# Performance work log

Hardware: AMD Instinct MI355X
Metric: run time of the kernel (lower is better)

## Reference

```python
import math
import jax, jax.numpy as jnp
import numpy as np

B, T, C, NH = 2, 2048, 2048, 16
HD = C // NH  # 128


def _quantize_int6(key, out_f, in_f):
    """Replicates Int6LinearDynamic.reset_parameters/_quantize_update."""
    w = jax.random.normal(key, (out_f, in_f), jnp.float32) * (1.0 / math.sqrt(in_f))
    max_val = jnp.clip(jnp.max(jnp.abs(w), axis=1, keepdims=True), 1e-5)
    scale = max_val / 31.0
    w_int = jnp.clip(jnp.round(w / scale), -32, 31).astype(jnp.int8)
    return w_int, scale.squeeze(1)  # [out,in] int8, [out] f32


def setup_inputs() -> dict:
    key = jax.random.key(0)
    k_x, k_a, k_p = jax.random.split(key, 3)
    attn_w, attn_scales = _quantize_int6(k_a, 3 * C, C)
    proj_w, proj_scales = _quantize_int6(k_p, C, C)
    return {
        "x": jax.random.normal(k_x, (B, T, C), jnp.float32),
        "attn_w": attn_w,
        "attn_scales": attn_scales,
        "proj_w": proj_w,
        "proj_scales": proj_scales,
        "qk_gain": jnp.float32(1.0),
    }


def _l2norm(t):
    # F.normalize(p=2, dim=-1, eps=1e-12)
    n = jnp.sqrt(jnp.sum(t * t, axis=-1, keepdims=True))
    return t / jnp.maximum(n, 1e-12)


def reference(x, attn_w, attn_scales, proj_w, proj_scales, qk_gain):
    # dequantized int6 GEMM: w = int8 * per-row scale
    wa = attn_w.astype(jnp.float32) * attn_scales[:, None]  # [3C, C]
    qkv = jnp.einsum("btc,oc->bto", x, wa)                   # [B,T,3C]
    q, k, v = jnp.split(qkv, 3, axis=2)

    def heads(t):  # [B,T,C] -> [B,NH,T,HD]
        return t.reshape(B, T, NH, HD).transpose(0, 2, 1, 3)

    q, k, v = heads(q), heads(k), heads(v)
    q = _l2norm(q) * qk_gain
    k = _l2norm(k) * qk_gain

    # causal SDPA, default scale 1/sqrt(head_dim)
    scores = jnp.einsum("bhqd,bhkd->bhqk", q, k) / math.sqrt(HD)
    causal = jnp.tril(jnp.ones((T, T), dtype=bool))
    scores = jnp.where(causal, scores, -jnp.inf)
    attn = jax.nn.softmax(scores, axis=-1)
    y = jnp.einsum("bhqk,bhkd->bhqd", attn, v)               # [B,NH,T,HD]
    y = y.transpose(0, 2, 1, 3).reshape(B, T, C)

    wp = proj_w.astype(jnp.float32) * proj_scales[:, None]   # [C, C]
    return jnp.einsum("btc,oc->bto", y, wp)
```

## Files before the change

kernel.cpp:

```cpp
#include <hip/hip_runtime.h>


#define DEVINL __device__ __forceinline__

typedef unsigned short u16;
typedef __bf16 bf16x8 __attribute__((ext_vector_type(8)));
typedef float  f32x4  __attribute__((ext_vector_type(4)));
typedef float  f32x16 __attribute__((ext_vector_type(16)));
typedef short  short8 __attribute__((ext_vector_type(8)));
typedef u16    u16x4  __attribute__((ext_vector_type(4)));
typedef unsigned uint4x __attribute__((ext_vector_type(4)));

static constexpr int T_  = 2048;
static constexpr int C_  = 2048;
static constexpr int TC3 = 6144;

DEVINL u16 f2bf(float f) {
  union { float f; unsigned u; } v; v.f = f;
  unsigned r = v.u + 0x7FFFu + ((v.u >> 16) & 1u);
  return (u16)(r >> 16);
}
DEVINL float bf2f(u16 s) {
  union { unsigned u; float f; } v; v.u = ((unsigned)s) << 16;
  return v.f;
}
DEVINL bf16x8 ld8(const u16* p) {
  return __builtin_bit_cast(bf16x8, *(const short8*)p);
}
DEVINL f32x4 mfma16(bf16x8 a, bf16x8 b, f32x4 c) {
  return __builtin_amdgcn_mfma_f32_16x16x32_bf16(a, b, c, 0, 0, 0);
}
DEVINL f32x16 mfma32(bf16x8 a, bf16x8 b, f32x16 c) {
  return __builtin_amdgcn_mfma_f32_32x32x16_bf16(a, b, c, 0, 0, 0);
}
DEVINL void async_cp16(const u16* gp, u16* lp) {
  __builtin_amdgcn_global_load_lds(
      (const __attribute__((address_space(1))) void*)gp,
      (__attribute__((address_space(3))) void*)lp, 16, 0, 0);
}
DEVINL unsigned cvtpk(float lo, float hi) {
  unsigned r;
  asm("v_cvt_pk_bf16_f32 %0, %1, %2" : "=v"(r) : "v"(lo), "v"(hi));
  return r;
}
DEVINL void plswap(unsigned& a, unsigned& b) {
  asm("v_permlane32_swap_b32 %0, %1" : "+v"(a), "+v"(b));
}
template<int N> DEVINL void vmwait() {
  if constexpr (N == 0)      asm volatile("s_waitcnt vmcnt(0)" ::: "memory");
  else if constexpr (N == 5) asm volatile("s_waitcnt vmcnt(5)" ::: "memory");
  else if constexpr (N == 7) asm volatile("s_waitcnt vmcnt(7)" ::: "memory");
  else if constexpr (N == 9) asm volatile("s_waitcnt vmcnt(9)" ::: "memory");
}

__global__ __launch_bounds__(256) void k_cast_x(const float* __restrict__ in,
                                                u16* __restrict__ out) {
  long i = (long)(blockIdx.x * 256 + threadIdx.x) * 4;
  float4 v = *(const float4*)(in + i);
  u16x4 o; o.x = f2bf(v.x); o.y = f2bf(v.y); o.z = f2bf(v.z); o.w = f2bf(v.w);
  *(u16x4*)(out + i) = o;
}
__global__ __launch_bounds__(256) void k_cast_w(const int* __restrict__ in,
                                                u16* __restrict__ out) {
  long i = (long)(blockIdx.x * 256 + threadIdx.x) * 4;
  int4 v = *(const int4*)(in + i);
  u16x4 o; o.x = f2bf((float)v.x); o.y = f2bf((float)v.y);
  o.z = f2bf((float)v.z); o.w = f2bf((float)v.w);
  *(u16x4*)(out + i) = o;
}

template<bool OUT_BF16>
__global__ __launch_bounds__(256) void k_gemm_bt(
    const u16* __restrict__ A, const u16* __restrict__ Bt,
    const float* __restrict__ scale, void* __restrict__ Cv,
    int N, long K) {
  __shared__ u16 As[128 * 32];
  __shared__ u16 Bs[128 * 32];
  const int tid  = threadIdx.x;
  const int wave = tid >> 6;
  const int lane = tid & 63;
  const int l15  = lane & 15;
  const int quad = lane >> 4;
  const int wm = (wave & 1) * 64;
  const int wn = (wave >> 1) * 64;
  const long bm = (long)blockIdx.y * 128;
  const long bn = (long)blockIdx.x * 128;

  f32x4 acc[4][4] = {};

  const int srow = lane >> 2;
  const int scol = (lane & 3) * 8;

  for (long k0 = 0; k0 < K; k0 += 32) {
#pragma unroll
    for (int i = 0; i < 2; ++i) {
      const int j = wave * 2 + i;
      const int row = j * 16 + srow;
      async_cp16(A  + (bm + row) * K + k0 + scol, &As[j * 512]);
      async_cp16(Bt + (bn + row) * K + k0 + scol, &Bs[j * 512]);
    }
    __syncthreads();
    bf16x8 af[4], bfr[4];
#pragma unroll
    for (int mi = 0; mi < 4; ++mi)
      af[mi] = ld8(&As[(wm + mi * 16 + l15) * 32 + quad * 8]);
#pragma unroll
    for (int ni = 0; ni < 4; ++ni)
      bfr[ni] = ld8(&Bs[(wn + ni * 16 + l15) * 32 + quad * 8]);
#pragma unroll
    for (int mi = 0; mi < 4; ++mi)
#pragma unroll
      for (int ni = 0; ni < 4; ++ni)
        acc[mi][ni] = mfma16(af[mi], bfr[ni], acc[mi][ni]);
    __syncthreads();
  }
#pragma unroll
  for (int ni = 0; ni < 4; ++ni) {
    const long col = bn + wn + ni * 16 + l15;
    const float sc = scale[col];
#pragma unroll
    for (int mi = 0; mi < 4; ++mi) {
      const long row0 = bm + wm + mi * 16 + quad * 4;
#pragma unroll
      for (int r = 0; r < 4; ++r) {
        float v = acc[mi][ni][r] * sc;
        if constexpr (OUT_BF16) ((u16*)Cv)[(row0 + r) * (long)N + col] = f2bf(v);
        else                    ((float*)Cv)[(row0 + r) * (long)N + col] = v;
      }
    }
  }
}

template<int SZ>
DEVINL void stage_q(const u16* __restrict__ G, long brow, long K, int tt, int qi,
                    u16 (&L)[2][SZ], int w, int lane) {
  const int sr = w * 8 + (lane >> 3);
  const int sc = lane & 7;
  const long grow = brow + qi * 64 + sr;
  async_cp16(G + grow * K + (long)(tt << 6) + ((sc ^ (sr & 7)) << 3),
             &L[tt & 1][(qi * 64 + w * 8) * 64]);
}

template<int WP1, int WP3, bool ISS0, bool ISS123, bool LAST>
DEVINL void kstep256(int t, const u16* __restrict__ A, const u16* __restrict__ Bt,
                     long K, long bm, long bn,
                     u16 (&As)[2][256 * 64], u16 (&Bs)[2][192 * 64],
                     f32x4 (&acc)[8][3], int w, int lane) {
  const int l15 = lane & 15, quad = lane >> 4;
  const int wm = (w & 1) * 128;
  const int wn = (w >> 1) * 48;
  const int buf = t & 1;

  auto rdA = [&](int mi, int kc) -> bf16x8 {
    const int row = wm + mi * 16 + l15;
    const int k0 = kc * 32 + quad * 8;
    return ld8(&As[buf][row * 64 + (k0 ^ ((row & 7) * 8))]);
  };
  auto rdB = [&](int ni, int kc) -> bf16x8 {
    const int row = wn + ni * 16 + l15;
    const int k0 = kc * 32 + quad * 8;
    return ld8(&Bs[buf][row * 64 + (k0 ^ ((row & 7) * 8))]);
  };

  bf16x8 af[4][2], bfl[2][2];
#pragma unroll
  for (int mi = 0; mi < 4; ++mi) { af[mi][0] = rdA(mi, 0); af[mi][1] = rdA(mi, 1); }
#pragma unroll
  for (int ni = 0; ni < 2; ++ni) { bfl[ni][0] = rdB(ni, 0); bfl[ni][1] = rdB(ni, 1); }
  if constexpr (ISS0) {
    stage_q(A, bm, K, t + 1, 1, As, w, lane);
    stage_q(A, bm, K, t + 1, 3, As, w, lane);
  }
  __builtin_amdgcn_s_barrier();
  __builtin_amdgcn_s_setprio(1);
#pragma unroll
  for (int mi = 0; mi < 4; ++mi)
#pragma unroll
    for (int ni = 0; ni < 2; ++ni) {
      acc[mi][ni] = mfma16(af[mi][0], bfl[ni][0], acc[mi][ni]);
      acc[mi][ni] = mfma16(af[mi][1], bfl[ni][1], acc[mi][ni]);
    }
  __builtin_amdgcn_s_setprio(0);
  __builtin_amdgcn_s_barrier();

  bf16x8 bfh[2];
  bfh[0] = rdB(2, 0); bfh[1] = rdB(2, 1);
  if constexpr (ISS123) {
    stage_q(A, bm, K, t + 2, 0, As, w, lane);
    stage_q(A, bm, K, t + 2, 2, As, w, lane);
  }
  __builtin_amdgcn_s_barrier();
  __builtin_amdgcn_s_setprio(1);
#pragma unroll
  for (int mi = 0; mi < 4; ++mi) {
    acc[mi][2] = mfma16(af[mi][0], bfh[0], acc[mi][2]);
    acc[mi][2] = mfma16(af[mi][1], bfh[1], acc[mi][2]);
  }
  __builtin_amdgcn_s_setprio(0);
  vmwait<WP1>();
  __builtin_amdgcn_s_barrier();

  bf16x8 af2[4][2];
#pragma unroll
  for (int mi = 0; mi < 4; ++mi) { af2[mi][0] = rdA(4 + mi, 0); af2[mi][1] = rdA(4 + mi, 1); }
  if constexpr (ISS123) {
    stage_q(Bt, bn, K, t + 2, 0, Bs, w, lane);
    stage_q(Bt, bn, K, t + 2, 1, Bs, w, lane);
  }
  __builtin_amdgcn_s_barrier();
  __builtin_amdgcn_s_setprio(1);
#pragma unroll
  for (int mi = 0; mi < 4; ++mi) {
    acc[4 + mi][2] = mfma16(af2[mi][0], bfh[0], acc[4 + mi][2]);
    acc[4 + mi][2] = mfma16(af2[mi][1], bfh[1], acc[4 + mi][2]);
  }
  __builtin_amdgcn_s_setprio(0);
  __builtin_amdgcn_s_barrier();

  if constexpr (ISS123) {
    stage_q(Bt, bn, K, t + 2, 2, Bs, w, lane);
  }
  __builtin_amdgcn_s_setprio(1);
#pragma unroll
  for (int mi = 0; mi < 4; ++mi)
#pragma unroll
    for (int ni = 0; ni < 2; ++ni) {
      acc[4 + mi][ni] = mfma16(af2[mi][0], bfl[ni][0], acc[4 + mi][ni]);
      acc[4 + mi][ni] = mfma16(af2[mi][1], bfl[ni][1], acc[4 + mi][ni]);
    }
  __builtin_amdgcn_s_setprio(0);
  if constexpr (!LAST) {
    vmwait<WP3>();
    __builtin_amdgcn_s_barrier();
  }
}

__global__ __launch_bounds__(512, 2) void k_gemm256(
    const u16* __restrict__ A, const u16* __restrict__ Bt,
    const float* __restrict__ scale, u16* __restrict__ C,
    int N, long K) {
  __shared__ u16 As[2][256 * 64];
  __shared__ u16 Bs[2][192 * 64];
  const int tid = threadIdx.x, w = tid >> 6, lane = tid & 63;
  const long bm = (long)blockIdx.y * 256;
  const long bn = (long)blockIdx.x * 192;
  const int nt = (int)(K >> 6);

  stage_q(A, bm, K, 0, 0, As, w, lane); stage_q(A, bm, K, 0, 2, As, w, lane);
  stage_q(Bt, bn, K, 0, 0, Bs, w, lane); stage_q(Bt, bn, K, 0, 1, Bs, w, lane);
  stage_q(Bt, bn, K, 0, 2, Bs, w, lane);
  stage_q(A, bm, K, 0, 1, As, w, lane); stage_q(A, bm, K, 0, 3, As, w, lane);
  stage_q(A, bm, K, 1, 0, As, w, lane); stage_q(A, bm, K, 1, 2, As, w, lane);
  stage_q(Bt, bn, K, 1, 0, Bs, w, lane); stage_q(Bt, bn, K, 1, 1, Bs, w, lane);
  stage_q(Bt, bn, K, 1, 2, Bs, w, lane);
  vmwait<5>();
  __builtin_amdgcn_s_barrier();

  f32x4 acc[8][3] = {};
  int t = 0;
  for (; t < nt - 2; ++t)
    kstep256<9, 5, true, true, false>(t, A, Bt, K, bm, bn, As, Bs, acc, w, lane);
  kstep256<7, 0, true, false, false>(nt - 2, A, Bt, K, bm, bn, As, Bs, acc, w, lane);
  kstep256<0, 0, false, false, true>(nt - 1, A, Bt, K, bm, bn, As, Bs, acc, w, lane);

  const int l15 = lane & 15, quad = lane >> 4;
  const int wm = (w & 1) * 128, wn = (w >> 1) * 48;
#pragma unroll
  for (int ni = 0; ni < 3; ++ni) {
    const long col = bn + wn + ni * 16 + l15;
    const float sc = scale[col];
#pragma unroll
    for (int mi = 0; mi < 8; ++mi) {
      const long row0 = bm + wm + mi * 16 + quad * 4;
#pragma unroll
      for (int r = 0; r < 4; ++r)
        C[(row0 + r) * (long)N + col] = f2bf(acc[mi][ni][r] * sc);
    }
  }
}

__global__ __launch_bounds__(256) void k_norm_qk(u16* __restrict__ qkv,
                                                 const float* __restrict__ qk_gain) {
  const int token = blockIdx.x;
  const int wave = threadIdx.x >> 6, lane = threadIdx.x & 63;
  const float g = qk_gain[0];
  const float qmul = g * g * 1.44269504f * 0.08838834764f;
  u16* rowp = qkv + (long)token * TC3;
#pragma unroll
  for (int s = 0; s < 8; ++s) {
    const int seg = wave * 8 + s;
    const int isK = seg >> 4;
    const int h = seg & 15;
    u16* ptr = rowp + isK * C_ + h * 128 + lane * 2;
    unsigned pv = *(const unsigned*)ptr;
    float a = bf2f((u16)(pv & 0xffffu));
    float bb = bf2f((u16)(pv >> 16));
    float ss = a * a + bb * bb;
#pragma unroll
    for (int m = 1; m <= 32; m <<= 1) ss += __shfl_xor(ss, m);
    float denom = fmaxf(sqrtf(ss), 1e-12f);
    float f = (isK ? 1.0f : qmul) / denom;
    u16 o0 = f2bf(a * f), o1 = f2bf(bb * f);
    *(unsigned*)ptr = (unsigned)o0 | ((unsigned)o1 << 16);
  }
}

__global__ __launch_bounds__(256) void k_vt(const u16* __restrict__ qkv,
                                            u16* __restrict__ vt) {
  const int t0 = blockIdx.x * 64;
  const int h = blockIdx.y, bz = blockIdx.z;
  const int t = threadIdx.x & 63;
  const int d0 = threadIdx.x >> 6;
  const long tokbase = (long)bz * T_;
  const u16* src = qkv + (tokbase + t0 + t) * (long)TC3 + 2 * C_ + h * 128;
  u16* dst = vt + ((long)(bz * 16 + h) * 128) * (long)T_ + t0 + t;
#pragma unroll
  for (int dd = 0; dd < 32; ++dd) {
    const int d = dd * 4 + d0;
    dst[(long)d * T_] = src[d];
  }
}

__global__ __launch_bounds__(256, 2) void k_attn(const u16* __restrict__ qkv,
                                                 const u16* __restrict__ vtg,
                                                 u16* __restrict__ y) {
  const int qt = blockIdx.z ? (15 - blockIdx.x) : blockIdx.x;
  const int h  = blockIdx.y;
  const int bz = blockIdx.z;
  const int tid = threadIdx.x, w = tid >> 6, lane = tid & 63;
  const int m31 = lane & 31, hi = lane >> 5;

  __shared__ u16 Ks[2][64 * 128];
  __shared__ u16 Vt[2][128 * 64];

  const long tokbase = (long)bz * T_;
  const int qbase = qt * 128 + w * 32;
  const u16* vbase = vtg + ((long)(bz * 16 + h) * 128) * (long)T_;
  const u16* kbase = qkv + tokbase * TC3 + C_ + h * 128;

  bf16x8 qf[8];
  {
    const u16* qp = qkv + (tokbase + qbase + m31) * (long)TC3 + h * 128 + hi * 8;
#pragma unroll
    for (int kc = 0; kc < 8; ++kc)
      qf[kc] = ld8(qp + kc * 16);
  }

  f32x16 o[4];
#pragma unroll
  for (int i = 0; i < 4; ++i)
#pragma unroll
    for (int r = 0; r < 16; ++r) o[i][r] = 0.f;
  f32x4 lacc = {0.f, 0.f, 0.f, 0.f};

  auto stage = [&](int ktb, int b) {
#pragma unroll
    for (int j = 0; j < 4; ++j) {
      const int t = w * 4 + j;
      const int p = t * 64 + lane;
      const int r  = p >> 4, ck = p & 15;
      async_cp16(kbase + (long)(ktb + r) * TC3 + ((ck ^ (r & 15)) * 8),
                 &Ks[b][t * 512]);
      const int d  = p >> 3, cv = p & 7;
      async_cp16(vbase + (long)d * T_ + ktb + ((cv ^ (d & 7)) * 8),
                 &Vt[b][t * 512]);
    }
  };

  stage(0, 0);
  __syncthreads();
  int b = 0;
  const int ktmax = 2 * qt + 1;

  for (int kt = 0; kt <= ktmax; ++kt) {
    const int ktb = kt * 64;
    if (kt < ktmax) stage(ktb + 64, b ^ 1);

    if (ktb <= qbase + 31) {
      f32x16 sA[2];
      __builtin_amdgcn_s_setprio(1);
#pragma unroll
      for (int kb = 0; kb < 2; ++kb) {
        f32x16 acc;
#pragma unroll
        for (int r = 0; r < 16; ++r) acc[r] = 0.f;
#pragma unroll
        for (int kc = 0; kc < 8; ++kc) {
          bf16x8 kf = ld8(&Ks[b][(kb * 32 + m31) * 128 +
                                 (((2 * kc + hi) ^ (lane & 15)) * 8)]);
          acc = mfma32(kf, qf[kc], acc);
        }
        sA[kb] = acc;
      }
      __builtin_amdgcn_s_setprio(0);

      if (ktb + 63 > qbase) {
        const int qq = qbase + m31;
#pragma unroll
        for (int kb = 0; kb < 2; ++kb)
#pragma unroll
          for (int r = 0; r < 16; ++r) {
            const int key = ktb + kb * 32 + (r & 3) + 8 * (r >> 2) + 4 * hi;
            if (key > qq) sA[kb][r] = -1e30f;
          }
      }
#pragma unroll
      for (int kb = 0; kb < 2; ++kb)
#pragma unroll
        for (int r = 0; r < 16; ++r) {
          float p = __builtin_amdgcn_exp2f(sA[kb][r]);
          sA[kb][r] = p;
          lacc[r & 3] += p;
        }

      bf16x8 pb[4];
#pragma unroll
      for (int ks = 0; ks < 4; ++ks) {
        const int kb = ks >> 1, j = ks & 1;
        unsigned w0a = cvtpk(sA[kb][8 * j + 0], sA[kb][8 * j + 1]);
        unsigned w1a = cvtpk(sA[kb][8 * j + 2], sA[kb][8 * j + 3]);
        unsigned w0b = cvtpk(sA[kb][8 * j + 4], sA[kb][8 * j + 5]);
        unsigned w1b = cvtpk(sA[kb][8 * j + 6], sA[kb][8 * j + 7]);
        plswap(w0a, w0b);
        plswap(w1a, w1b);
        uint4x t; t.x = w0a; t.y = w1a; t.z = w0b; t.w = w1b;
        pb[ks] = __builtin_bit_cast(bf16x8, t);
      }

      __builtin_amdgcn_s_setprio(1);
#pragma unroll
      for (int db = 0; db < 4; ++db)
#pragma unroll
        for (int ks = 0; ks < 4; ++ks) {
          bf16x8 vf = ld8(&Vt[b][(db * 32 + m31) * 64 +
                                 (((2 * ks + hi) ^ (m31 & 7)) * 8)]);
          o[db] = mfma32(vf, pb[ks], o[db]);
        }
      __builtin_amdgcn_s_setprio(0);
    }

    if (kt < ktmax) __syncthreads();
    b ^= 1;
  }

  float lrow = lacc[0] + lacc[1] + lacc[2] + lacc[3];
  lrow += __shfl_xor(lrow, 32);
  const float inv_l = 1.0f / lrow;
  u16* yp = y + (tokbase + qbase + m31) * (long)C_ + h * 128 + 4 * hi;
#pragma unroll
  for (int db = 0; db < 4; ++db)
#pragma unroll
    for (int g = 0; g < 4; ++g) {
      u16x4 pk;
#pragma unroll
      for (int r = 0; r < 4; ++r) pk[r] = f2bf(o[db][g * 4 + r] * inv_l);
      *(u16x4*)(yp + db * 32 + g * 8) = pk;
    }
}

extern "C" void kernel_launch(void* const* d_in, const int* in_sizes, int n_in,
                              void* d_out, int out_size, void* d_ws, size_t ws_size,
                              hipStream_t stream) {
  const float* x    = (const float*)d_in[0];
  const int*   aw   = (const int*)d_in[1];
  const float* asc  = (const float*)d_in[2];
  const int*   pw   = (const int*)d_in[3];
  const float* psc  = (const float*)d_in[4];
  const float* gain = (const float*)d_in[5];

  char* ws = (char*)d_ws;
  u16* xb  = (u16*)(ws);
  u16* wab = (u16*)(ws + 16777216UL);
  u16* wpb = (u16*)(ws + 41943040UL);
  u16* qkv = (u16*)(ws + 50331648UL);
  u16* yb  = (u16*)(ws + 100663296UL);
  u16* vtg = xb;

  k_cast_x<<<8192, 256, 0, stream>>>(x, xb);
  k_cast_w<<<12288, 256, 0, stream>>>(aw, wab);
  k_cast_w<<<4096, 256, 0, stream>>>(pw, wpb);
  k_gemm256<<<dim3(32, 16), 512, 0, stream>>>(xb, wab, asc, qkv, TC3, (long)C_);
  k_norm_qk<<<4096, 256, 0, stream>>>(qkv, gain);
  k_vt<<<dim3(32, 16, 2), 256, 0, stream>>>(qkv, vtg);
  k_attn<<<dim3(16, 16, 2), 256, 0, stream>>>(qkv, vtg, yb);
  k_gemm_bt<false><<<dim3(16, 32), 256, 0, stream>>>(yb, wpb, psc, (float*)d_out, C_, (long)C_);
}
```

Baseline: 419.4 us.

## Merge cast and norm/transpose launches; add pipelined 128x256 projection GEMM

Folds the three cast kernels into one launch and the q/k normalisation and V transpose into another, cutting launch count. It also replaces the simple 128x128, K=32 projection GEMM with a 512-thread, 128x256-tile kernel. The new kernel double-buffers 64-wide K slices in swizzled LDS via async copies and interleaves MFMA sub-blocks with barriers and setprio. The costs are more LDS per block (96 KB, double-buffered) and a more complex barrier schedule.

New measurement: 416.3 us. Within noise of the previous version (-0.7%).

```diff
diff --git a/kernel.cpp b/kernel.cpp
--- a/kernel.cpp
+++ b/kernel.cpp
@@ -53,81 +53,25 @@
   else if constexpr (N == 9) asm volatile("s_waitcnt vmcnt(9)" ::: "memory");
 }
 
-__global__ __launch_bounds__(256) void k_cast_x(const float* __restrict__ in,
-                                                u16* __restrict__ out) {
-  long i = (long)(blockIdx.x * 256 + threadIdx.x) * 4;
-  float4 v = *(const float4*)(in + i);
-  u16x4 o; o.x = f2bf(v.x); o.y = f2bf(v.y); o.z = f2bf(v.z); o.w = f2bf(v.w);
-  *(u16x4*)(out + i) = o;
-}
-__global__ __launch_bounds__(256) void k_cast_w(const int* __restrict__ in,
-                                                u16* __restrict__ out) {
-  long i = (long)(blockIdx.x * 256 + threadIdx.x) * 4;
-  int4 v = *(const int4*)(in + i);
-  u16x4 o; o.x = f2bf((float)v.x); o.y = f2bf((float)v.y);
-  o.z = f2bf((float)v.z); o.w = f2bf((float)v.w);
-  *(u16x4*)(out + i) = o;
-}
-
-template<bool OUT_BF16>
-__global__ __launch_bounds__(256) void k_gemm_bt(
-    const u16* __restrict__ A, const u16* __restrict__ Bt,
-    const float* __restrict__ scale, void* __restrict__ Cv,
-    int N, long K) {
-  __shared__ u16 As[128 * 32];
-  __shared__ u16 Bs[128 * 32];
-  const int tid  = threadIdx.x;
-  const int wave = tid >> 6;
-  const int lane = tid & 63;
-  const int l15  = lane & 15;
-  const int quad = lane >> 4;
-  const int wm = (wave & 1) * 64;
-  const int wn = (wave >> 1) * 64;
-  const long bm = (long)blockIdx.y * 128;
-  const long bn = (long)blockIdx.x * 128;
-
-  f32x4 acc[4][4] = {};
-
-  const int srow = lane >> 2;
-  const int scol = (lane & 3) * 8;
-
-  for (long k0 = 0; k0 < K; k0 += 32) {
-#pragma unroll
-    for (int i = 0; i < 2; ++i) {
-      const int j = wave * 2 + i;
-      const int row = j * 16 + srow;
-      async_cp16(A  + (bm + row) * K + k0 + scol, &As[j * 512]);
-      async_cp16(Bt + (bn + row) * K + k0 + scol, &Bs[j * 512]);
-    }
-    __syncthreads();
-    bf16x8 af[4], bfr[4];
-#pragma unroll
-    for (int mi = 0; mi < 4; ++mi)
-      af[mi] = ld8(&As[(wm + mi * 16 + l15) * 32 + quad * 8]);
-#pragma unroll
-    for (int ni = 0; ni < 4; ++ni)
-      bfr[ni] = ld8(&Bs[(wn + ni * 16 + l15) * 32 + quad * 8]);
-#pragma unroll
-    for (int mi = 0; mi < 4; ++mi)
-#pragma unroll
-      for (int ni = 0; ni < 4; ++ni)
-        acc[mi][ni] = mfma16(af[mi], bfr[ni], acc[mi][ni]);
-    __syncthreads();
-  }
-#pragma unroll
-  for (int ni = 0; ni < 4; ++ni) {
-    const long col = bn + wn + ni * 16 + l15;
-    const float sc = scale[col];
-#pragma unroll
-    for (int mi = 0; mi < 4; ++mi) {
-      const long row0 = bm + wm + mi * 16 + quad * 4;
-#pragma unroll
-      for (int r = 0; r < 4; ++r) {
-        float v = acc[mi][ni][r] * sc;
-        if constexpr (OUT_BF16) ((u16*)Cv)[(row0 + r) * (long)N + col] = f2bf(v);
-        else                    ((float*)Cv)[(row0 + r) * (long)N + col] = v;
-      }
-    }
+__global__ __launch_bounds__(256) void k_cast_all(
+    const float* __restrict__ x, const int* __restrict__ aw,
+    const int* __restrict__ pw, u16* __restrict__ xb,
+    u16* __restrict__ wab, u16* __restrict__ wpb) {
+  const int b = blockIdx.x;
+  if (b < 8192) {
+    long i = (long)(b * 256 + threadIdx.x) * 4;
+    float4 v = *(const float4*)(x + i);
+    u16x4 o; o.x = f2bf(v.x); o.y = f2bf(v.y); o.z = f2bf(v.z); o.w = f2bf(v.w);
+    *(u16x4*)(xb + i) = o;
+  } else {
+    const int* in; u16* out; int lb;
+    if (b < 20480) { in = aw; out = wab; lb = b - 8192; }
+    else           { in = pw; out = wpb; lb = b - 20480; }
+    long i = (long)(lb * 256 + threadIdx.x) * 4;
+    int4 v = *(const int4*)(in + i);
+    u16x4 o; o.x = f2bf((float)v.x); o.y = f2bf((float)v.y);
+    o.z = f2bf((float)v.z); o.w = f2bf((float)v.w);
+    *(u16x4*)(out + i) = o;
   }
 }
 
@@ -279,45 +223,167 @@
   }
 }
 
-__global__ __launch_bounds__(256) void k_norm_qk(u16* __restrict__ qkv,
-                                                 const float* __restrict__ qk_gain) {
-  const int token = blockIdx.x;
-  const int wave = threadIdx.x >> 6, lane = threadIdx.x & 63;
-  const float g = qk_gain[0];
-  const float qmul = g * g * 1.44269504f * 0.08838834764f;
-  u16* rowp = qkv + (long)token * TC3;
-#pragma unroll
-  for (int s = 0; s < 8; ++s) {
-    const int seg = wave * 8 + s;
-    const int isK = seg >> 4;
-    const int h = seg & 15;
-    u16* ptr = rowp + isK * C_ + h * 128 + lane * 2;
-    unsigned pv = *(const unsigned*)ptr;
-    float a = bf2f((u16)(pv & 0xffffu));
-    float bb = bf2f((u16)(pv >> 16));
-    float ss = a * a + bb * bb;
-#pragma unroll
-    for (int m = 1; m <= 32; m <<= 1) ss += __shfl_xor(ss, m);
-    float denom = fmaxf(sqrtf(ss), 1e-12f);
-    float f = (isK ? 1.0f : qmul) / denom;
-    u16 o0 = f2bf(a * f), o1 = f2bf(bb * f);
-    *(unsigned*)ptr = (unsigned)o0 | ((unsigned)o1 << 16);
-  }
-}
-
-__global__ __launch_bounds__(256) void k_vt(const u16* __restrict__ qkv,
-                                            u16* __restrict__ vt) {
-  const int t0 = blockIdx.x * 64;
-  const int h = blockIdx.y, bz = blockIdx.z;
-  const int t = threadIdx.x & 63;
-  const int d0 = threadIdx.x >> 6;
-  const long tokbase = (long)bz * T_;
-  const u16* src = qkv + (tokbase + t0 + t) * (long)TC3 + 2 * C_ + h * 128;
-  u16* dst = vt + ((long)(bz * 16 + h) * 128) * (long)T_ + t0 + t;
-#pragma unroll
-  for (int dd = 0; dd < 32; ++dd) {
-    const int d = dd * 4 + d0;
-    dst[(long)d * T_] = src[d];
+__global__ __launch_bounds__(512, 2) void k_gemm_proj(
+    const u16* __restrict__ A, const u16* __restrict__ Bt,
+    const float* __restrict__ scale, float* __restrict__ C,
+    int N, long K) {
+  __shared__ u16 As[2][128 * 64];
+  __shared__ u16 Bs[2][256 * 64];
+  const int tid = threadIdx.x, w = tid >> 6, lane = tid & 63;
+  const int l15 = lane & 15, quad = lane >> 4;
+  const int wm = (w & 1) * 64, wn = (w >> 1) * 64;
+  const long bm = (long)blockIdx.y * 128;
+  const long bn = (long)blockIdx.x * 256;
+  const int nt = (int)(K >> 6);
+
+  auto rdA = [&](int mi, int kc, int buf) -> bf16x8 {
+    const int row = wm + mi * 16 + l15;
+    const int k0 = kc * 32 + quad * 8;
+    return ld8(&As[buf][row * 64 + (k0 ^ ((row & 7) * 8))]);
+  };
+  auto rdB = [&](int ni, int kc, int buf) -> bf16x8 {
+    const int row = wn + ni * 16 + l15;
+    const int k0 = kc * 32 + quad * 8;
+    return ld8(&Bs[buf][row * 64 + (k0 ^ ((row & 7) * 8))]);
+  };
+
+  stage_q(A, bm, K, 0, 0, As, w, lane); stage_q(A, bm, K, 0, 1, As, w, lane);
+  stage_q(Bt, bn, K, 0, 0, Bs, w, lane); stage_q(Bt, bn, K, 0, 1, Bs, w, lane);
+  stage_q(Bt, bn, K, 0, 2, Bs, w, lane); stage_q(Bt, bn, K, 0, 3, Bs, w, lane);
+  vmwait<0>();
+  __builtin_amdgcn_s_barrier();
+
+  f32x4 acc[4][4] = {};
+  for (int t = 0; t < nt; ++t) {
+    const int buf = t & 1;
+    const bool iss = (t < nt - 1);
+    bf16x8 a01[2][2], a23[2][2], b01[2][2], b23[2][2];
+
+    if (iss) {
+      stage_q(Bt, bn, K, t + 1, 0, Bs, w, lane);
+      stage_q(Bt, bn, K, t + 1, 1, Bs, w, lane);
+      stage_q(A,  bm, K, t + 1, 0, As, w, lane);
+    }
+#pragma unroll
+    for (int mi = 0; mi < 2; ++mi) { a01[mi][0] = rdA(mi, 0, buf); a01[mi][1] = rdA(mi, 1, buf); }
+#pragma unroll
+    for (int ni = 0; ni < 2; ++ni) { b01[ni][0] = rdB(ni, 0, buf); b01[ni][1] = rdB(ni, 1, buf); }
+    __builtin_amdgcn_s_barrier();
+    __builtin_amdgcn_s_setprio(1);
+#pragma unroll
+    for (int mi = 0; mi < 2; ++mi)
+#pragma unroll
+      for (int ni = 0; ni < 2; ++ni) {
+        acc[mi][ni] = mfma16(a01[mi][0], b01[ni][0], acc[mi][ni]);
+        acc[mi][ni] = mfma16(a01[mi][1], b01[ni][1], acc[mi][ni]);
+      }
+    __builtin_amdgcn_s_setprio(0);
+    __builtin_amdgcn_s_barrier();
+
+    if (iss) {
+      stage_q(Bt, bn, K, t + 1, 2, Bs, w, lane);
+      stage_q(Bt, bn, K, t + 1, 3, Bs, w, lane);
+      stage_q(A,  bm, K, t + 1, 1, As, w, lane);
+    }
+#pragma unroll
+    for (int ni = 0; ni < 2; ++ni) { b23[ni][0] = rdB(2 + ni, 0, buf); b23[ni][1] = rdB(2 + ni, 1, buf); }
+    __builtin_amdgcn_s_barrier();
+    __builtin_amdgcn_s_setprio(1);
+#pragma unroll
+    for (int mi = 0; mi < 2; ++mi)
+#pragma unroll
+      for (int ni = 0; ni < 2; ++ni) {
+        acc[mi][2 + ni] = mfma16(a01[mi][0], b23[ni][0], acc[mi][2 + ni]);
+        acc[mi][2 + ni] = mfma16(a01[mi][1], b23[ni][1], acc[mi][2 + ni]);
+      }
+    __builtin_amdgcn_s_setprio(0);
+    __builtin_amdgcn_s_barrier();
+
+#pragma unroll
+    for (int mi = 0; mi < 2; ++mi) { a23[mi][0] = rdA(2 + mi, 0, buf); a23[mi][1] = rdA(2 + mi, 1, buf); }
+    __builtin_amdgcn_s_barrier();
+    __builtin_amdgcn_s_setprio(1);
+#pragma unroll
+    for (int mi = 0; mi < 2; ++mi)
+#pragma unroll
+      for (int ni = 0; ni < 2; ++ni) {
+        acc[2 + mi][2 + ni] = mfma16(a23[mi][0], b23[ni][0], acc[2 + mi][2 + ni]);
+        acc[2 + mi][2 + ni] = mfma16(a23[mi][1], b23[ni][1], acc[2 + mi][2 + ni]);
+      }
+    __builtin_amdgcn_s_setprio(0);
+    __builtin_amdgcn_s_barrier();
+
+    __builtin_amdgcn_s_setprio(1);
+#pragma unroll
+    for (int mi = 0; mi < 2; ++mi)
+#pragma unroll
+      for (int ni = 0; ni < 2; ++ni) {
+        acc[2 + mi][ni] = mfma16(a23[mi][0], b01[ni][0], acc[2 + mi][ni]);
+        acc[2 + mi][ni] = mfma16(a23[mi][1], b01[ni][1], acc[2 + mi][ni]);
+      }
+    __builtin_amdgcn_s_setprio(0);
+    if (iss) {
+      vmwait<0>();
+      __builtin_amdgcn_s_barrier();
+    }
+  }
+
+#pragma unroll
+  for (int ni = 0; ni < 4; ++ni) {
+    const long col = bn + wn + ni * 16 + l15;
+    const float sc = scale[col];
+#pragma unroll
+    for (int mi = 0; mi < 4; ++mi) {
+      const long row0 = bm + wm + mi * 16 + quad * 4;
+#pragma unroll
+      for (int r = 0; r < 4; ++r)
+        C[(row0 + r) * (long)N + col] = acc[mi][ni][r] * sc;
+    }
+  }
+}
+
+__global__ __launch_bounds__(256) void k_norm_vt(u16* __restrict__ qkv,
+                                                 const float* __restrict__ qk_gain,
+                                                 u16* __restrict__ vt) {
+  const int b = blockIdx.x;
+  if (b < 4096) {
+    const int token = b;
+    const int wave = threadIdx.x >> 6, lane = threadIdx.x & 63;
+    const float g = qk_gain[0];
+    const float qmul = g * g * 1.44269504f * 0.08838834764f;
+    u16* rowp = qkv + (long)token * TC3;
+#pragma unroll
+    for (int s = 0; s < 8; ++s) {
+      const int seg = wave * 8 + s;
+      const int isK = seg >> 4;
+      const int h = seg & 15;
+      u16* ptr = rowp + isK * C_ + h * 128 + lane * 2;
+      unsigned pv = *(const unsigned*)ptr;
+      float a = bf2f((u16)(pv & 0xffffu));
+      float bb = bf2f((u16)(pv >> 16));
+      float ss = a * a + bb * bb;
+#pragma unroll
+      for (int m = 1; m <= 32; m <<= 1) ss += __shfl_xor(ss, m);
+      float denom = fmaxf(sqrtf(ss), 1e-12f);
+      float f = (isK ? 1.0f : qmul) / denom;
+      u16 o0 = f2bf(a * f), o1 = f2bf(bb * f);
+      *(unsigned*)ptr = (unsigned)o0 | ((unsigned)o1 << 16);
+    }
+  } else {
+    const int v = b - 4096;
+    const int t0 = (v & 31) * 64;
+    const int h = (v >> 5) & 15;
+    const int bz = v >> 9;
+    const int t = threadIdx.x & 63;
+    const int d0 = threadIdx.x >> 6;
+    const long tokbase = (long)bz * T_;
+    const u16* src = qkv + (tokbase + t0 + t) * (long)TC3 + 2 * C_ + h * 128;
+    u16* dst = vt + ((long)(bz * 16 + h) * 128) * (long)T_ + t0 + t;
+#pragma unroll
+    for (int dd = 0; dd < 32; ++dd) {
+      const int d = dd * 4 + d0;
+      dst[(long)d * T_] = src[d];
+    }
   }
 }
 
@@ -353,17 +419,17 @@
     for (int r = 0; r < 16; ++r) o[i][r] = 0.f;
   f32x4 lacc = {0.f, 0.f, 0.f, 0.f};
 
-  auto stage = [&](int ktb, int b) {
+  auto stage = [&](int ktb, int b2) {
 #pragma unroll
     for (int j = 0; j < 4; ++j) {
       const int t = w * 4 + j;
       const int p = t * 64 + lane;
       const int r  = p >> 4, ck = p & 15;
       async_cp16(kbase + (long)(ktb + r) * TC3 + ((ck ^ (r & 15)) * 8),
-                 &Ks[b][t * 512]);
+                 &Ks[b2][t * 512]);
       const int d  = p >> 3, cv = p & 7;
       async_cp16(vbase + (long)d * T_ + ktb + ((cv ^ (d & 7)) * 8),
-                 &Vt[b][t * 512]);
+                 &Vt[b2][t * 512]);
     }
   };
 
@@ -476,12 +542,9 @@
   u16* yb  = (u16*)(ws + 100663296UL);
   u16* vtg = xb;
 
-  k_cast_x<<<8192, 256, 0, stream>>>(x, xb);
-  k_cast_w<<<12288, 256, 0, stream>>>(aw, wab);
-  k_cast_w<<<4096, 256, 0, stream>>>(pw, wpb);
+  k_cast_all<<<24576, 256, 0, stream>>>(x, aw, pw, xb, wab, wpb);
   k_gemm256<<<dim3(32, 16), 512, 0, stream>>>(xb, wab, asc, qkv, TC3, (long)C_);
-  k_norm_qk<<<4096, 256, 0, stream>>>(qkv, gain);
-  k_vt<<<dim3(32, 16, 2), 256, 0, stream>>>(qkv, vtg);
+  k_norm_vt<<<5120, 256, 0, stream>>>(qkv, gain, vtg);
   k_attn<<<dim3(16, 16, 2), 256, 0, stream>>>(qkv, vtg, yb);
-  k_gemm_bt<false><<<dim3(16, 32), 256, 0, stream>>>(yb, wpb, psc, (float*)d_out, C_, (long)C_);
-}
+  k_gemm_proj<<<dim3(8, 32), 512, 0, stream>>>(yb, wpb, psc, (float*)d_out, C_, (long)C_);
+}
```
